# Performance work log

Hardware: AMD Instinct MI355X
Metric: run time of the kernel (lower is better)

## Reference

```python
import jax, jax.numpy as jnp
import numpy as np

BN_EPS = 1e-5

def knn_indices(loc, new_loc, k):
    # squared distances [B, M, N] via ||y||^2 + ||x||^2 - 2 y.x (no [B,M,N,3] materialization)
    x2 = jnp.sum(loc * loc, axis=-1)          # [B, N]
    y2 = jnp.sum(new_loc * new_loc, axis=-1)  # [B, M]
    d2 = y2[:, :, None] + x2[:, None, :] - 2.0 * jnp.einsum('bmc,bnc->bmn', new_loc, loc)
    _, idx = jax.lax.top_k(-d2, k)            # smallest-k -> [B, M, K]
    return idx

def gather_neighbors(x, idx):
    # x [B, N, C], idx [B, M, K] -> [B, M, K, C]
    return jax.vmap(lambda xb, ib: xb[ib])(x, idx)

def conv_bn_relu(x, W, g, b):
    # x [B, Cin, M, K]; 1x1 conv (no bias) + training-mode BatchNorm2d + ReLU
    y = jnp.einsum('oc,bcmk->bomk', W, x)
    mu = jnp.mean(y, axis=(0, 2, 3), keepdims=True)
    var = jnp.var(y, axis=(0, 2, 3), keepdims=True)  # biased, as torch BN uses for normalization
    y = (y - mu) * jax.lax.rsqrt(var + BN_EPS)
    return jax.nn.relu(y * g[None, :, None, None] + b[None, :, None, None])

def setup_inputs() -> dict:
    key = jax.random.key(0)
    ks = jax.random.split(key, 8)
    B, N, M, C = 16, 4096, 1024, 64
    loc = jax.random.normal(ks[0], (B, N, 3), dtype=jnp.float32)
    new_loc = jax.random.normal(ks[1], (B, M, 3), dtype=jnp.float32)
    features = jax.random.normal(ks[2], (B, C, N), dtype=jnp.float32)
    W1 = jax.random.normal(ks[3], (64, 67), dtype=jnp.float32) * (1.0 / np.sqrt(67.0))
    W2 = jax.random.normal(ks[4], (64, 64), dtype=jnp.float32) * (1.0 / np.sqrt(64.0))
    W3 = jax.random.normal(ks[5], (128, 64), dtype=jnp.float32) * (1.0 / np.sqrt(64.0))
    return {
        'loc': loc, 'new_loc': new_loc, 'features': features,
        'W1': W1, 'g1': jnp.ones(64, jnp.float32), 'b1': jnp.zeros(64, jnp.float32),
        'W2': W2, 'g2': jnp.ones(64, jnp.float32), 'b2': jnp.zeros(64, jnp.float32),
        'W3': W3, 'g3': jnp.ones(128, jnp.float32), 'b3': jnp.zeros(128, jnp.float32),
    }

def reference(loc, new_loc, features, W1, g1, b1, W2, g2, b2, W3, g3, b3):
    K = 32
    idx = knn_indices(loc, new_loc, K)                      # [B, M, K]
    knn_loc = gather_neighbors(loc, idx)                    # [B, M, K, 3]
    knn_loc = jnp.transpose(knn_loc, (0, 3, 1, 2))          # [B, 3, M, K]
    knn_loc = knn_loc - jnp.transpose(new_loc, (0, 2, 1))[..., None]  # relative xyz
    knn_feat = gather_neighbors(jnp.transpose(features, (0, 2, 1)), idx)  # [B, M, K, C]
    knn_feat = jnp.transpose(knn_feat, (0, 3, 1, 2))        # [B, C, M, K]
    h = jnp.concatenate([knn_loc, knn_feat], axis=1)        # [B, C+3, M, K]
    h = conv_bn_relu(h, W1, g1, b1)
    h = conv_bn_relu(h, W2, g2, b2)
    h = conv_bn_relu(h, W3, g3, b3)
    return jnp.max(h, axis=3)                               # [B, 128, M]
```

## Files before the change

kernel.cpp:

```cpp
#include <hip/hip_runtime.h>
#include <stdint.h>

#define B_   16
#define N_   4096
#define M_   1024
#define NT   (B_*M_*32)
#define BM   (B_*M_)
#define REP  64

typedef unsigned short u16;
typedef unsigned long long u64;
typedef __attribute__((ext_vector_type(8))) short short8;
typedef __attribute__((ext_vector_type(4))) float f32x4;

union FragU { uint4 u; short8 s; };

__device__ __forceinline__ float bf2f(u16 u){
    return __uint_as_float(((unsigned int)u) << 16);
}
__device__ __forceinline__ u16 f2bf(float f){
    unsigned int u = __float_as_uint(f);
    return (u16)((u + 0x7FFFu + ((u >> 16) & 1u)) >> 16);
}

__global__ __launch_bounds__(256) void k_feat(const float* __restrict__ feat,
                                              float* __restrict__ featT){
    __shared__ float tile[64][65];
    int b  = blockIdx.y;
    int n0 = blockIdx.x * 64;
    for (int t = threadIdx.x; t < 4096; t += 256){
        int c = t >> 6, n = t & 63;
        tile[c][n] = feat[((size_t)(b*64 + c))*N_ + n0 + n];
    }
    __syncthreads();
    for (int t = threadIdx.x; t < 4096; t += 256){
        int n = t >> 6, c = t & 63;
        featT[((size_t)(b*N_) + n0 + n)*64 + c] = tile[c][n];
    }
}

__global__ __launch_bounds__(256) void k_prep(const float* __restrict__ locF,
                                              float4* __restrict__ locP){
    int i = blockIdx.x*256 + threadIdx.x;
    float lx = locF[(size_t)i*3+0], ly = locF[(size_t)i*3+1], lz = locF[(size_t)i*3+2];
    float x2 = __fadd_rn(__fadd_rn(__fmul_rn(lx,lx), __fmul_rn(ly,ly)), __fmul_rn(lz,lz));
    locP[i] = make_float4(lx, ly, lz, x2);
}

__global__ __launch_bounds__(256) void k_knn(const float4* __restrict__ locP,
                                             const float* __restrict__ nlocF,
                                             int* __restrict__ idxOut){
    const int tid  = threadIdx.x;
    const int lane = tid & 63, wv = tid >> 6;
    const int q    = blockIdx.x;
    const int b    = q >> 10, m = q & 1023;

    float qx = nlocF[(size_t)(b*M_ + m)*3 + 0];
    float qy = nlocF[(size_t)(b*M_ + m)*3 + 1];
    float qz = nlocF[(size_t)(b*M_ + m)*3 + 2];
    float y2 = __fadd_rn(__fadd_rn(__fmul_rn(qx,qx), __fmul_rn(qy,qy)), __fmul_rn(qz,qz));

    unsigned int key[16];
    const float4* lb = locP + (size_t)b*N_;
    #pragma unroll
    for (int i = 0; i < 16; ++i){
        int n = i*256 + tid;
        float4 p = lb[n];
        float dt = __fadd_rn(__fadd_rn(__fmul_rn(qx,p.x), __fmul_rn(qy,p.y)), __fmul_rn(qz,p.z));
        float d2 = __fsub_rn(__fadd_rn(y2, p.w), __fmul_rn(2.0f, dt));
        d2 = fmaxf(d2, 0.0f);
        key[i] = __float_as_uint(d2);
    }

    __shared__ unsigned int hist[4][256];
    __shared__ float wmm[4][2];
    __shared__ u64 cand[128];
    __shared__ int sOut[32];
    __shared__ int outCnt, candCnt;

    float lmin = 3.4e38f, lmax = 0.0f;
    #pragma unroll
    for (int i = 0; i < 16; ++i){
        float kf = __uint_as_float(key[i]);
        lmin = fminf(lmin, kf); lmax = fmaxf(lmax, kf);
    }
    #pragma unroll
    for (int st = 1; st < 64; st <<= 1){
        lmin = fminf(lmin, __shfl_xor(lmin, st, 64));
        lmax = fmaxf(lmax, __shfl_xor(lmax, st, 64));
    }
    if (tid == 0){ outCnt = 0; candCnt = 0; }
    if (lane == 0){ wmm[wv][0] = lmin; wmm[wv][1] = lmax; }
    __syncthreads();
    float lo = fminf(fminf(wmm[0][0], wmm[1][0]), fminf(wmm[2][0], wmm[3][0]));
    float hi = fmaxf(fmaxf(wmm[0][1], wmm[1][1]), fmaxf(wmm[2][1], wmm[3][1]));

    unsigned int act = 0xFFFFu;
    int bkt[16];
    int R = 32;

    for (int lvl = 0; lvl < 8; ++lvl){
        float scale = 255.0f / fmaxf(hi - lo, 1e-35f);
        ((uint4*)hist)[tid] = make_uint4(0,0,0,0);
        __syncthreads();
        #pragma unroll
        for (int i = 0; i < 16; ++i){
            if (act & (1u << i)){
                float kf = __uint_as_float(key[i]);
                int bb = (int)((kf - lo) * scale);
                bb = bb < 0 ? 0 : (bb > 255 ? 255 : bb);
                bkt[i] = bb;
                atomicAdd(&hist[wv][bb], 1u);
            }
        }
        __syncthreads();
        uint4 ha = *(const uint4*)&hist[0][lane << 2];
        uint4 hb = *(const uint4*)&hist[1][lane << 2];
        uint4 hc = *(const uint4*)&hist[2][lane << 2];
        uint4 hd = *(const uint4*)&hist[3][lane << 2];
        uint4 h = make_uint4(ha.x+hb.x+hc.x+hd.x, ha.y+hb.y+hc.y+hd.y,
                             ha.z+hb.z+hc.z+hd.z, ha.w+hb.w+hc.w+hd.w);
        int tot = (int)(h.x + h.y + h.z + h.w);
        int v = tot;
        #pragma unroll
        for (int st = 1; st < 64; st <<= 1){
            int u = __shfl_up(v, st, 64);
            if (lane >= st) v += u;
        }
        u64 bal = __ballot(v >= R);
        int Ls = __ffsll((unsigned long long)bal) - 1;
        int exclS = __shfl(v - tot, Ls, 64);
        int hx = __shfl((int)h.x, Ls, 64), hy = __shfl((int)h.y, Ls, 64);
        int hz = __shfl((int)h.z, Ls, 64), hw = __shfl((int)h.w, Ls, 64);
        int c0 = exclS + hx, c1 = c0 + hy, c2 = c1 + hz;
        int jj    = (c0 >= R) ? 0 : (c1 >= R) ? 1 : (c2 >= R) ? 2 : 3;
        int below = (jj == 0) ? exclS : (jj == 1) ? c0 : (jj == 2) ? c1 : c2;
        int cnt   = (jj == 0) ? hx : (jj == 1) ? hy : (jj == 2) ? hz : hw;
        int qb = Ls*4 + jj;
        R -= below;
        bool brk = (cnt <= 128) || (lvl == 7);

        float nlo = 3.4e38f, nhi = 0.0f;
        #pragma unroll
        for (int i = 0; i < 16; ++i){
            if (act & (1u << i)){
                int bb = bkt[i];
                if (bb < qb){
                    int pos = atomicAdd(&outCnt, 1);
                    if (pos < 32) sOut[pos] = i*256 + tid;
                    act &= ~(1u << i);
                } else if (bb > qb){
                    act &= ~(1u << i);
                } else if (!brk){
                    float kf = __uint_as_float(key[i]);
                    nlo = fminf(nlo, kf); nhi = fmaxf(nhi, kf);
                }
            }
        }
        if (brk) break;
        #pragma unroll
        for (int st = 1; st < 64; st <<= 1){
            nlo = fminf(nlo, __shfl_xor(nlo, st, 64));
            nhi = fmaxf(nhi, __shfl_xor(nhi, st, 64));
        }
        __syncthreads();
        if (lane == 0){ wmm[wv][0] = nlo; wmm[wv][1] = nhi; }
        __syncthreads();
        lo = fminf(fminf(wmm[0][0], wmm[1][0]), fminf(wmm[2][0], wmm[3][0]));
        hi = fmaxf(fmaxf(wmm[0][1], wmm[1][1]), fmaxf(wmm[2][1], wmm[3][1]));
    }

    #pragma unroll
    for (int i = 0; i < 16; ++i){
        if (act & (1u << i)){
            int pos = atomicAdd(&candCnt, 1);
            if (pos < 128) cand[pos] = (((u64)key[i]) << 32) | (unsigned int)(i*256 + tid);
        }
    }
    __syncthreads();
    int c = candCnt < 128 ? candCnt : 128;
    int base = outCnt;
    if (tid < c){
        u64 me = cand[tid];
        int rank = 0;
        for (int j = 0; j < c; ++j) rank += (cand[j] < me) ? 1 : 0;
        if (rank < R) sOut[base + rank] = (int)(me & 0xFFFFFFFFull);
    }
    __syncthreads();
    if (tid < 32) idxOut[(size_t)q*32 + tid] = sOut[tid];
}

__global__ __launch_bounds__(256) void k_conv1m(const int* __restrict__ idx,
                                                const float* __restrict__ locF,
                                                const float* __restrict__ nlocF,
                                                const float* __restrict__ featT,
                                                const float* __restrict__ W1,
                                                u16* __restrict__ y1,
                                                float* __restrict__ gsum,
                                                float* __restrict__ gsq){
    __shared__ uint4 bfB[4*5*64];
    __shared__ u16  tileT[64*136];
    __shared__ float sSum[64], sSq[64];
    const int t   = threadIdx.x;
    const int bid = blockIdx.x;
    const int rep = bid & (REP-1);
    const int swz = (bid & 7)*512 + (bid >> 3);
    const int s0  = swz * 128;
    const int b   = s0 >> 15;

    if (t < 64){ sSum[t] = 0.0f; sSq[t] = 0.0f; }

    #pragma unroll
    for (int rp = 0; rp < 5; ++rp){
        int cid = rp*256 + t;
        int ln  = cid & 63;
        int kk  = (cid >> 6) % 5;
        int nt  = cid / 320;
        int o   = nt*16 + (ln & 15);
        int qq  = ln >> 4;
        int cb  = kk*16 + qq*4;
        unsigned int d[4];
        #pragma unroll
        for (int h = 0; h < 4; ++h){
            int c = cb + h;
            float wv = (c < 64) ? W1[o*67 + 3 + c] : ((c < 67) ? W1[o*67 + (c - 64)] : 0.0f);
            unsigned int wh = (unsigned int)f2bf(wv);
            d[h] = wh | (wh << 16);
        }
        bfB[cid] = make_uint4(d[0], d[1], d[2], d[3]);
    }

    const int w = t >> 6, lane = t & 63;
    const int m15 = lane & 15, q = lane >> 4;

    int nrow[2], sg[2];
    float4 fa[2][4];
    #pragma unroll
    for (int mt = 0; mt < 2; ++mt){
        int sl = (2*w + mt)*16 + m15;
        sg[mt] = s0 + sl;
        int n = idx[sg[mt]]; if ((unsigned)n >= N_) n = 0;
        nrow[mt] = n;
        const float4* fp = (const float4*)&featT[((size_t)(b*N_) + n)*64];
        #pragma unroll
        for (int kq = 0; kq < 4; ++kq)
            fa[mt][kq] = fp[kq*4 + q];
    }
    uint4 axyz[2];
    axyz[0] = make_uint4(0,0,0,0); axyz[1] = make_uint4(0,0,0,0);
    if (q == 0){
        #pragma unroll
        for (int mt = 0; mt < 2; ++mt){
            int n = nrow[mt];
            int m = (sg[mt] >> 5) & 1023;
            const float* lp = &locF[(size_t)(b*N_ + n)*3];
            const float* qp = &nlocF[(size_t)(b*M_ + m)*3];
            unsigned int dd[3];
            #pragma unroll
            for (int e = 0; e < 3; ++e){
                float r  = lp[e] - qp[e];
                u16 hi   = f2bf(r);
                float lo = r - bf2f(hi);
                dd[e] = (unsigned int)hi | (((unsigned int)f2bf(lo)) << 16);
            }
            axyz[mt] = make_uint4(dd[0], dd[1], dd[2], 0u);
        }
    }
    __syncthreads();

    f32x4 acc[2][4];
    #pragma unroll
    for (int mt = 0; mt < 2; ++mt)
        #pragma unroll
        for (int nt = 0; nt < 4; ++nt)
            acc[mt][nt] = (f32x4){0.0f, 0.0f, 0.0f, 0.0f};

    #pragma unroll
    for (int kk = 0; kk < 5; ++kk){
        FragU af[2];
        #pragma unroll
        for (int mt = 0; mt < 2; ++mt){
            if (kk < 4){
                float4 f = fa[mt][kk];
                float fv[4] = {f.x, f.y, f.z, f.w};
                unsigned int d[4];
                #pragma unroll
                for (int e = 0; e < 4; ++e){
                    u16 hi   = f2bf(fv[e]);
                    float lo = fv[e] - bf2f(hi);
                    d[e] = (unsigned int)hi | (((unsigned int)f2bf(lo)) << 16);
                }
                af[mt].u = make_uint4(d[0], d[1], d[2], d[3]);
            } else {
                af[mt].u = axyz[mt];
            }
        }
        #pragma unroll
        for (int nt = 0; nt < 4; ++nt){
            FragU bu; bu.u = bfB[(nt*5 + kk)*64 + lane];
            #pragma unroll
            for (int mt = 0; mt < 2; ++mt)
                acc[mt][nt] = __builtin_amdgcn_mfma_f32_16x16x32_bf16(af[mt].s, bu.s, acc[mt][nt], 0, 0, 0);
        }
    }

    {
        float st4[4], sq4[4];
        #pragma unroll
        for (int nt = 0; nt < 4; ++nt){ st4[nt] = 0.0f; sq4[nt] = 0.0f; }
        #pragma unroll
        for (int mt = 0; mt < 2; ++mt)
            #pragma unroll
            for (int nt = 0; nt < 4; ++nt){
                f32x4 a = acc[mt][nt];
                st4[nt] += (a[0] + a[1]) + (a[2] + a[3]);
                float qv = a[0]*a[0];
                qv = fmaf(a[1], a[1], qv); qv = fmaf(a[2], a[2], qv); qv = fmaf(a[3], a[3], qv);
                sq4[nt] += qv;
            }
        #pragma unroll
        for (int st = 16; st < 64; st <<= 1){
            #pragma unroll
            for (int nt = 0; nt < 4; ++nt){
                st4[nt] += __shfl_xor(st4[nt], st, 64);
                sq4[nt] += __shfl_xor(sq4[nt], st, 64);
            }
        }
        if (lane < 16){
            #pragma unroll
            for (int nt = 0; nt < 4; ++nt){
                atomicAdd(&sSum[nt*16 + lane], st4[nt]);
                atomicAdd(&sSq[nt*16 + lane],  sq4[nt]);
            }
        }
    }

    #pragma unroll
    for (int mt = 0; mt < 2; ++mt){
        int s_base = w*32 + mt*16 + (lane >> 4)*4;
        #pragma unroll
        for (int nt = 0; nt < 4; ++nt){
            int o = nt*16 + (lane & 15);
            f32x4 a = acc[mt][nt];
            unsigned int p01 = (unsigned int)f2bf(a[0]) | (((unsigned int)f2bf(a[1])) << 16);
            unsigned int p23 = (unsigned int)f2bf(a[2]) | (((unsigned int)f2bf(a[3])) << 16);
            *(unsigned int*)&tileT[o*136 + s_base]     = p01;
            *(unsigned int*)&tileT[o*136 + s_base + 2] = p23;
        }
    }
    __syncthreads();

    {
        int c  = t >> 2;
        int g0 = (t & 3)*32;
        #pragma unroll
        for (int j = 0; j < 4; ++j){
            uint4 v = *(const uint4*)&tileT[c*136 + g0 + j*8];
            *(uint4*)&y1[(size_t)c*NT + s0 + g0 + j*8] = v;
        }
    }
    if (t < 64){
        atomicAdd(&gsum[rep*64 + t], sSum[t]);
        atomicAdd(&gsq[rep*64 + t],  sSq[t]);
    }
}

__global__ __launch_bounds__(256) void k_conv2m(const u16* __restrict__ yin,
                                                const float* __restrict__ W2,
                                                const float* __restrict__ prm,
                                                u16* __restrict__ yout,
                                                float* __restrict__ gsum,
                                                float* __restrict__ gsq){
    __shared__ uint4 bfA[2048];
    __shared__ uint4 bfB[512];
    __shared__ u16  tileT[64*264];
    __shared__ float sS[64], sT[64];
    __shared__ float sSum[64], sSq[64];
    const int t   = threadIdx.x;
    const int rep = blockIdx.x & (REP-1);
    const int s0  = blockIdx.x * 256;

    if (t < 64){ sS[t] = prm[t]; sT[t] = prm[64 + t]; sSum[t] = 0.0f; sSq[t] = 0.0f; }
    __syncthreads();

    #pragma unroll
    for (int rp = 0; rp < 2; ++rp){
        int cid = rp*256 + t;
        int ln  = cid & 63;
        int kk  = (cid >> 6) & 1;
        int nt  = cid >> 7;
        int o   = nt*16 + (ln & 15);
        int k0  = kk*32 + (ln >> 4)*8;
        const float* wp = &W2[o*64 + k0];
        unsigned int d[4];
        #pragma unroll
        for (int h = 0; h < 4; ++h)
            d[h] = (unsigned int)f2bf(wp[2*h]) | (((unsigned int)f2bf(wp[2*h+1])) << 16);
        bfB[cid] = make_uint4(d[0], d[1], d[2], d[3]);
    }

    {
        int oct = t >> 5;
        int sg  = t & 31;
        int c0  = oct*8;
        int kk  = oct >> 2;
        int qd  = oct & 3;
        u16 rb[8][8];
        #pragma unroll
        for (int j = 0; j < 8; ++j){
            int c = c0 + j;
            uint4 pk = *(const uint4*)&yin[(size_t)c*NT + s0 + sg*8];
            float sc = sS[c], tb = sT[c];
            unsigned int w4[4] = {pk.x, pk.y, pk.z, pk.w};
            #pragma unroll
            for (int h = 0; h < 4; ++h){
                rb[j][2*h]   = f2bf(fmaxf(fmaf(bf2f((u16)(w4[h] & 0xFFFF)), sc, tb), 0.0f));
                rb[j][2*h+1] = f2bf(fmaxf(fmaf(bf2f((u16)(w4[h] >> 16)),   sc, tb), 0.0f));
            }
        }
        #pragma unroll
        for (int i = 0; i < 8; ++i){
            int s   = sg*8 + i;
            int mtg = s >> 4, m15 = s & 15;
            int l64 = qd*16 + m15;
            int cb  = (mtg*2 + kk)*64 + (l64 ^ (mtg & 7));
            unsigned int d[4];
            #pragma unroll
            for (int h = 0; h < 4; ++h)
                d[h] = (unsigned int)rb[2*h][i] | (((unsigned int)rb[2*h+1][i]) << 16);
            bfA[cb] = make_uint4(d[0], d[1], d[2], d[3]);
        }
    }
    __syncthreads();

    const int w = t >> 6, lane = t & 63;
    f32x4 acc[4][4];
    #pragma unroll
    for (int mt = 0; mt < 4; ++mt)
        #pragma unroll
        for (int nt = 0; nt < 4; ++nt)
            acc[mt][nt] = (f32x4){0.0f, 0.0f, 0.0f, 0.0f};

    #pragma unroll
    for (int kk = 0; kk < 2; ++kk){
        short8 af[4];
        #pragma unroll
        for (int mt = 0; mt < 4; ++mt){
            int tile = 4*w + mt;
            af[mt] = *((const short8*)&bfA[(tile*2 + kk)*64 + (lane ^ (tile & 7))]);
        }
        #pragma unroll
        for (int nt = 0; nt < 4; ++nt){
            short8 bfr = *((const short8*)&bfB[(nt*2 + kk)*64 + lane]);
            #pragma unroll
            for (int mt = 0; mt < 4; ++mt)
                acc[mt][nt] = __builtin_amdgcn_mfma_f32_16x16x32_bf16(af[mt], bfr, acc[mt][nt], 0, 0, 0);
        }
    }

    {
        float st4[4], sq4[4];
        #pragma unroll
        for (int nt = 0; nt < 4; ++nt){ st4[nt] = 0.0f; sq4[nt] = 0.0f; }
        #pragma unroll
        for (int mt = 0; mt < 4; ++mt)
            #pragma unroll
            for (int nt = 0; nt < 4; ++nt){
                f32x4 a = acc[mt][nt];
                st4[nt] += (a[0] + a[1]) + (a[2] + a[3]);
                float qq = a[0]*a[0];
                qq = fmaf(a[1], a[1], qq); qq = fmaf(a[2], a[2], qq); qq = fmaf(a[3], a[3], qq);
                sq4[nt] += qq;
            }
        #pragma unroll
        for (int st = 16; st < 64; st <<= 1){
            #pragma unroll
            for (int nt = 0; nt < 4; ++nt){
                st4[nt] += __shfl_xor(st4[nt], st, 64);
                sq4[nt] += __shfl_xor(sq4[nt], st, 64);
            }
        }
        if (lane < 16){
            #pragma unroll
            for (int nt = 0; nt < 4; ++nt){
                atomicAdd(&sSum[nt*16 + lane], st4[nt]);
                atomicAdd(&sSq[nt*16 + lane],  sq4[nt]);
            }
        }
    }

    #pragma unroll
    for (int mt = 0; mt < 4; ++mt){
        int s_base = w*64 + mt*16 + (lane >> 4)*4;
        #pragma unroll
        for (int nt = 0; nt < 4; ++nt){
            int o = nt*16 + (lane & 15);
            f32x4 a = acc[mt][nt];
            unsigned int p01 = (unsigned int)f2bf(a[0]) | (((unsigned int)f2bf(a[1])) << 16);
            unsigned int p23 = (unsigned int)f2bf(a[2]) | (((unsigned int)f2bf(a[3])) << 16);
            *(unsigned int*)&tileT[o*264 + s_base]     = p01;
            *(unsigned int*)&tileT[o*264 + s_base + 2] = p23;
        }
    }
    __syncthreads();

    {
        int c  = t >> 2;
        int g0 = (t & 3)*8;
        #pragma unroll
        for (int j = 0; j < 8; ++j){
            uint4 v = *(const uint4*)&tileT[c*264 + (g0 + j)*8];
            *(uint4*)&yout[(size_t)c*NT + s0 + (g0 + j)*8] = v;
        }
    }
    if (t < 64){
        atomicAdd(&gsum[rep*64 + t], sSum[t]);
        atomicAdd(&gsq[rep*64 + t],  sSq[t]);
    }
}

__global__ __launch_bounds__(256) void k_conv3m(const u16* __restrict__ yin,
                                                const float* __restrict__ W3,
                                                const float* __restrict__ prm,
                                                float* __restrict__ gsum, float* __restrict__ gsq,
                                                float* __restrict__ gmax, float* __restrict__ gmin){
    __shared__ uint4 bfA[2048];
    __shared__ uint4 bfB[1024];
    __shared__ float sS[64], sT[64];
    __shared__ float sSum[128], sSq[128];
    const int t   = threadIdx.x;
    const int rep = blockIdx.x & (REP-1);
    const int s0  = blockIdx.x * 256;

    if (t < 64){ sS[t] = prm[t]; sT[t] = prm[64 + t]; }
    if (t < 128){ sSum[t] = 0.0f; sSq[t] = 0.0f; }
    __syncthreads();

    #pragma unroll
    for (int rp = 0; rp < 4; ++rp){
        int cid = rp*256 + t;
        int ln  = cid & 63;
        int kk  = (cid >> 6) & 1;
        int nt  = cid >> 7;
        int o   = nt*16 + (ln & 15);
        int k0  = kk*32 + (ln >> 4)*8;
        const float* wp = &W3[o*64 + k0];
        unsigned int d[4];
        #pragma unroll
        for (int h = 0; h < 4; ++h)
            d[h] = (unsigned int)f2bf(wp[2*h]) | (((unsigned int)f2bf(wp[2*h+1])) << 16);
        bfB[cid] = make_uint4(d[0], d[1], d[2], d[3]);
    }

    {
        int oct = t >> 5;
        int sg  = t & 31;
        int c0  = oct*8;
        int kk  = oct >> 2;
        int qd  = oct & 3;
        u16 rb[8][8];
        #pragma unroll
        for (int j = 0; j < 8; ++j){
            int c = c0 + j;
            uint4 pk = *(const uint4*)&yin[(size_t)c*NT + s0 + sg*8];
            float sc = sS[c], tb = sT[c];
            unsigned int w4[4] = {pk.x, pk.y, pk.z, pk.w};
            #pragma unroll
            for (int h = 0; h < 4; ++h){
                rb[j][2*h]   = f2bf(fmaxf(fmaf(bf2f((u16)(w4[h] & 0xFFFF)), sc, tb), 0.0f));
                rb[j][2*h+1] = f2bf(fmaxf(fmaf(bf2f((u16)(w4[h] >> 16)),   sc, tb), 0.0f));
            }
        }
        #pragma unroll
        for (int i = 0; i < 8; ++i){
            int s   = sg*8 + i;
            int mtg = s >> 4, m15 = s & 15;
            int l64 = qd*16 + m15;
            int cb  = (mtg*2 + kk)*64 + (l64 ^ (mtg & 7));
            unsigned int d[4];
            #pragma unroll
            for (int h = 0; h < 4; ++h)
                d[h] = (unsigned int)rb[2*h][i] | (((unsigned int)rb[2*h+1][i]) << 16);
            bfA[cb] = make_uint4(d[0], d[1], d[2], d[3]);
        }
    }
    __syncthreads();

    const int w = t >> 6, lane = t & 63;
    f32x4 acc[4][8];
    #pragma unroll
    for (int mt = 0; mt < 4; ++mt)
        #pragma unroll
        for (int nt = 0; nt < 8; ++nt)
            acc[mt][nt] = (f32x4){0.0f, 0.0f, 0.0f, 0.0f};

    #pragma unroll
    for (int kk = 0; kk < 2; ++kk){
        short8 af[4];
        #pragma unroll
        for (int mt = 0; mt < 4; ++mt){
            int tile = 4*w + mt;
            af[mt] = *((const short8*)&bfA[(tile*2 + kk)*64 + (lane ^ (tile & 7))]);
        }
        #pragma unroll
        for (int nt = 0; nt < 8; ++nt){
            short8 bfr = *((const short8*)&bfB[(nt*2 + kk)*64 + lane]);
            #pragma unroll
            for (int mt = 0; mt < 4; ++mt)
                acc[mt][nt] = __builtin_amdgcn_mfma_f32_16x16x32_bf16(af[mt], bfr, acc[mt][nt], 0, 0, 0);
        }
    }

    float stS[8], stQ[8];
    #pragma unroll
    for (int nt = 0; nt < 8; ++nt){ stS[nt] = 0.0f; stQ[nt] = 0.0f; }

    #pragma unroll
    for (int g = 0; g < 2; ++g){
        const size_t gg = (size_t)(blockIdx.x*8 + w*2 + g);
        #pragma unroll
        for (int nt = 0; nt < 8; ++nt){
            f32x4 a0 = acc[2*g][nt], a1 = acc[2*g+1][nt];
            float mx = fmaxf(fmaxf(fmaxf(a0[0], a0[1]), fmaxf(a0[2], a0[3])),
                             fmaxf(fmaxf(a1[0], a1[1]), fmaxf(a1[2], a1[3])));
            float mn = fminf(fminf(fminf(a0[0], a0[1]), fminf(a0[2], a0[3])),
                             fminf(fminf(a1[0], a1[1]), fminf(a1[2], a1[3])));
            float sm = (a0[0]+a0[1]) + (a0[2]+a0[3]) + (a1[0]+a1[1]) + (a1[2]+a1[3]);
            float sq = a0[0]*a0[0];
            sq = fmaf(a0[1], a0[1], sq); sq = fmaf(a0[2], a0[2], sq); sq = fmaf(a0[3], a0[3], sq);
            sq = fmaf(a1[0], a1[0], sq); sq = fmaf(a1[1], a1[1], sq); sq = fmaf(a1[2], a1[2], sq);
            sq = fmaf(a1[3], a1[3], sq);
            #pragma unroll
            for (int st = 16; st < 64; st <<= 1){
                mx = fmaxf(mx, __shfl_xor(mx, st, 64));
                mn = fminf(mn, __shfl_xor(mn, st, 64));
                sm += __shfl_xor(sm, st, 64);
                sq += __shfl_xor(sq, st, 64);
            }
            if (lane < 16){
                gmax[gg*128 + nt*16 + lane] = mx;
                gmin[gg*128 + nt*16 + lane] = mn;
            }
            stS[nt] += sm; stQ[nt] += sq;
        }
    }
    if (lane < 16){
        #pragma unroll
        for (int nt = 0; nt < 8; ++nt){
            atomicAdd(&sSum[nt*16 + lane], stS[nt]);
            atomicAdd(&sSq[nt*16 + lane],  stQ[nt]);
        }
    }
    __syncthreads();
    if (t < 128){
        atomicAdd(&gsum[rep*128 + t], sSum[t]);
        atomicAdd(&gsq[rep*128 + t],  sSq[t]);
    }
}

__global__ void k_fold(const float* __restrict__ sum, const float* __restrict__ sumsq,
                       const float* __restrict__ gW, const float* __restrict__ bW,
                       float* __restrict__ prm, int C){
    int c = threadIdx.x;
    if (c < C){
        float s = 0.0f, q = 0.0f;
        for (int r = 0; r < REP; ++r){
            s += sum[r*C + c];
            q += sumsq[r*C + c];
        }
        const float inv = 1.0f / (float)NT;
        float mu  = s * inv;
        float var = q * inv - mu*mu;
        float sc  = gW[c] / sqrtf(var + 1e-5f);
        prm[c]     = sc;
        prm[C + c] = bW[c] - mu*sc;
    }
}

__global__ __launch_bounds__(256) void k_final(const float* __restrict__ gmax,
                                               const float* __restrict__ gmin,
                                               const float* __restrict__ prm,
                                               float* __restrict__ out){
    int bo = blockIdx.y;
    int b = bo >> 7, o = bo & 127;
    int m = blockIdx.x*256 + threadIdx.x;
    float sc = prm[o], tt = prm[128 + o];
    size_t i = (size_t)(b*M_ + m)*128 + o;
    float v = (sc >= 0.0f) ? gmax[i] : gmin[i];
    out[((size_t)(b*128 + o))*M_ + m] = fmaxf(fmaf(v, sc, tt), 0.0f);
}

extern "C" void kernel_launch(void* const* d_in, const int* in_sizes, int n_in,
                              void* d_out, int out_size, void* d_ws, size_t ws_size,
                              hipStream_t stream){
    const float* loc  = (const float*)d_in[0];
    const float* nloc = (const float*)d_in[1];
    const float* feat = (const float*)d_in[2];
    const float* W1   = (const float*)d_in[3];
    const float* g1   = (const float*)d_in[4];
    const float* b1   = (const float*)d_in[5];
    const float* W2   = (const float*)d_in[6];
    const float* g2   = (const float*)d_in[7];
    const float* b2   = (const float*)d_in[8];
    const float* W3   = (const float*)d_in[9];
    const float* g3   = (const float*)d_in[10];
    const float* b3   = (const float*)d_in[11];
    float* out = (float*)d_out;

    char* ws = (char*)d_ws;
    float* prm1  = (float*)(ws + 2048);
    float* prm2  = (float*)(ws + 2048 + 512);
    float* prm3  = (float*)(ws + 2048 + 1024);
    int*   idx   = (int*)(ws + 4096);
    float* gmax  = (float*)(ws + 2101248);
    float* gmin  = (float*)(ws + 10489856);
    float* featT = (float*)(ws + 18878464);
    u16*   y1    = (u16*)(ws + 35655680);
    u16*   y2    = (u16*)(ws + 102764544);
    float4* locP = (float4*)gmax;
    float* rep12 = (float*)(ws + 2101248 + 1048576);
    float* sum1 = rep12;
    float* sq1  = rep12 + REP*64;
    float* sum2 = rep12 + 2*REP*64;
    float* sq2  = rep12 + 3*REP*64;
    float* rep3 = (float*)featT;
    float* sum3 = rep3;
    float* sq3  = rep3 + REP*128;

    hipMemsetAsync(rep12, 0, 4*REP*64*sizeof(float), stream);

    k_feat<<<dim3(N_/64, B_), 256, 0, stream>>>(feat, featT);
    k_prep<<<(B_*N_)/256, 256, 0, stream>>>(loc, locP);
    k_knn<<<B_*M_, 256, 0, stream>>>(locP, nloc, idx);

    k_conv1m<<<NT/128, 256, 0, stream>>>(idx, loc, nloc, featT, W1, y1, sum1, sq1);
    k_fold<<<1, 128, 0, stream>>>(sum1, sq1, g1, b1, prm1, 64);
    hipMemsetAsync(rep3, 0, 2*REP*128*sizeof(float), stream);

    k_conv2m<<<NT/256, 256, 0, stream>>>(y1, W2, prm1, y2, sum2, sq2);
    k_fold<<<1, 128, 0, stream>>>(sum2, sq2, g2, b2, prm2, 64);

    k_conv3m<<<NT/256, 256, 0, stream>>>(y2, W3, prm2, sum3, sq3, gmax, gmin);
    k_fold<<<1, 128, 0, stream>>>(sum3, sq3, g3, b3, prm3, 128);

    k_final<<<dim3(M_/256, B_*128), 256, 0, stream>>>(gmax, gmin, prm3, out);
}
```

Measured before the change: 380.4 us.

## Use radix-byte selection for kNN and tile-transpose the final output kernel

The kNN top-k selection drops its adaptive float-range histogram, which needed min/max reductions and extra barriers at every level, and instead buckets the non-negative float bit patterns one byte at a time from the top (radix select), capped at four levels. The final kernel now stages a 32x128 tile in shared memory so that both the gathered reads of gmax/gmin and the transposed output writes are coalesced. The radix scheme may take more levels when distances cluster inside a single exponent byte, and may leave more than 128 candidates at the last level.

```diff
diff --git a/kernel.cpp b/kernel.cpp
--- a/kernel.cpp
+++ b/kernel.cpp
@@ -73,42 +73,23 @@
     }
 
     __shared__ unsigned int hist[4][256];
-    __shared__ float wmm[4][2];
     __shared__ u64 cand[128];
     __shared__ int sOut[32];
     __shared__ int outCnt, candCnt;
 
-    float lmin = 3.4e38f, lmax = 0.0f;
-    #pragma unroll
-    for (int i = 0; i < 16; ++i){
-        float kf = __uint_as_float(key[i]);
-        lmin = fminf(lmin, kf); lmax = fmaxf(lmax, kf);
-    }
-    #pragma unroll
-    for (int st = 1; st < 64; st <<= 1){
-        lmin = fminf(lmin, __shfl_xor(lmin, st, 64));
-        lmax = fmaxf(lmax, __shfl_xor(lmax, st, 64));
-    }
     if (tid == 0){ outCnt = 0; candCnt = 0; }
-    if (lane == 0){ wmm[wv][0] = lmin; wmm[wv][1] = lmax; }
-    __syncthreads();
-    float lo = fminf(fminf(wmm[0][0], wmm[1][0]), fminf(wmm[2][0], wmm[3][0]));
-    float hi = fmaxf(fmaxf(wmm[0][1], wmm[1][1]), fmaxf(wmm[2][1], wmm[3][1]));
 
     unsigned int act = 0xFFFFu;
     int bkt[16];
     int R = 32;
 
-    for (int lvl = 0; lvl < 8; ++lvl){
-        float scale = 255.0f / fmaxf(hi - lo, 1e-35f);
+    for (int shift = 24; shift >= 0; shift -= 8){
         ((uint4*)hist)[tid] = make_uint4(0,0,0,0);
         __syncthreads();
         #pragma unroll
         for (int i = 0; i < 16; ++i){
             if (act & (1u << i)){
-                float kf = __uint_as_float(key[i]);
-                int bb = (int)((kf - lo) * scale);
-                bb = bb < 0 ? 0 : (bb > 255 ? 255 : bb);
+                int bb = (int)((key[i] >> shift) & 255u);
                 bkt[i] = bb;
                 atomicAdd(&hist[wv][bb], 1u);
             }
@@ -138,9 +119,8 @@
         int cnt   = (jj == 0) ? hx : (jj == 1) ? hy : (jj == 2) ? hz : hw;
         int qb = Ls*4 + jj;
         R -= below;
-        bool brk = (cnt <= 128) || (lvl == 7);
-
-        float nlo = 3.4e38f, nhi = 0.0f;
+        bool brk = (cnt <= 128) || (shift == 0);
+
         #pragma unroll
         for (int i = 0; i < 16; ++i){
             if (act & (1u << i)){
@@ -151,23 +131,11 @@
                     act &= ~(1u << i);
                 } else if (bb > qb){
                     act &= ~(1u << i);
-                } else if (!brk){
-                    float kf = __uint_as_float(key[i]);
-                    nlo = fminf(nlo, kf); nhi = fmaxf(nhi, kf);
                 }
             }
         }
         if (brk) break;
-        #pragma unroll
-        for (int st = 1; st < 64; st <<= 1){
-            nlo = fminf(nlo, __shfl_xor(nlo, st, 64));
-            nhi = fmaxf(nhi, __shfl_xor(nhi, st, 64));
-        }
         __syncthreads();
-        if (lane == 0){ wmm[wv][0] = nlo; wmm[wv][1] = nhi; }
-        __syncthreads();
-        lo = fminf(fminf(wmm[0][0], wmm[1][0]), fminf(wmm[2][0], wmm[3][0]));
-        hi = fmaxf(fmaxf(wmm[0][1], wmm[1][1]), fmaxf(wmm[2][1], wmm[3][1]));
     }
 
     #pragma unroll
@@ -681,13 +649,30 @@
                                                const float* __restrict__ gmin,
                                                const float* __restrict__ prm,
                                                float* __restrict__ out){
-    int bo = blockIdx.y;
-    int b = bo >> 7, o = bo & 127;
-    int m = blockIdx.x*256 + threadIdx.x;
-    float sc = prm[o], tt = prm[128 + o];
-    size_t i = (size_t)(b*M_ + m)*128 + o;
-    float v = (sc >= 0.0f) ? gmax[i] : gmin[i];
-    out[((size_t)(b*128 + o))*M_ + m] = fmaxf(fmaf(v, sc, tt), 0.0f);
+    __shared__ float tile[32][129];
+    __shared__ float sS[128], sT[128];
+    const int t   = threadIdx.x;
+    const int blk = blockIdx.x;
+    const int b   = blk >> 5;
+    const int m0  = (blk & 31) * 32;
+    if (t < 128){ sS[t] = prm[t]; sT[t] = prm[128 + t]; }
+    __syncthreads();
+    #pragma unroll
+    for (int i = 0; i < 16; ++i){
+        int v  = i*256 + t;
+        int ml = v >> 7, o = v & 127;
+        float sc = sS[o];
+        size_t gi = (size_t)(b*M_ + m0 + ml)*128 + o;
+        float val = (sc >= 0.0f) ? gmax[gi] : gmin[gi];
+        tile[ml][o] = fmaxf(fmaf(val, sc, sT[o]), 0.0f);
+    }
+    __syncthreads();
+    #pragma unroll
+    for (int i = 0; i < 16; ++i){
+        int v  = i*256 + t;
+        int o  = v >> 5, ml = v & 31;
+        out[((size_t)(b*128 + o))*M_ + m0 + ml] = tile[ml][o];
+    }
 }
 
 extern "C" void kernel_launch(void* const* d_in, const int* in_sizes, int n_in,
@@ -743,5 +728,5 @@
     k_conv3m<<<NT/256, 256, 0, stream>>>(y2, W3, prm2, sum3, sq3, gmax, gmin);
     k_fold<<<1, 128, 0, stream>>>(sum3, sq3, g3, b3, prm3, 128);
 
-    k_final<<<dim3(M_/256, B_*128), 256, 0, stream>>>(gmax, gmin, prm3, out);
-}
+    k_final<<<dim3(B_*32), 256, 0, stream>>>(gmax, gmin, prm3, out);
+}
```

Result: slower. 463.7 us (+21.9%).
